# Optimization experiments

Measured on AMD Instinct MI355X. Metric: run time of the kernel, lower is better.

The kernel has to match this reference:

```python
import jax, jax.numpy as jnp
import numpy as np

B, C, H, W = 8, 96, 256, 256
PATCH, DIM, HEAD = 2, 384, 4
D = DIM // HEAD          # 96, minGRU feature dim
K = 2 * PATCH + 1        # 5, patch-embed kernel
GK = 3                   # positional conv kernel


def setup_inputs() -> dict:
    key = jax.random.key(0)
    ks = jax.random.split(key, 16)
    w = lambda k, shape: jax.random.normal(k, shape, jnp.float32) * 0.02
    return {
        'x': jax.random.normal(ks[0], (B, C, H, W), jnp.float32),
        'r_pw': w(ks[1], (DIM, C, K, K)),            # Conv2d weight (out,in,kh,kw)
        'r_pb': w(ks[2], (DIM,)),
        'c_pw': w(ks[3], (DIM, C, K, K)),
        'c_pb': w(ks[4], (DIM,)),
        'r_pe_w': w(ks[5], (DIM, DIM // C, GK, GK)),  # grouped conv, groups=C
        'r_pe_b': w(ks[6], (DIM,)),
        'c_pe_w': w(ks[7], (DIM, DIM // C, GK, GK)),
        'c_pe_b': w(ks[8], (DIM,)),
        'r_un_w': w(ks[9], (DIM, C, PATCH, PATCH)),   # ConvTranspose2d weight (in,out,kh,kw)
        'r_un_b': w(ks[10], (C,)),
        'c_un_w': w(ks[11], (DIM, C, PATCH, PATCH)),
        'c_un_b': w(ks[12], (C,)),
        'r_gru_w': w(ks[13], (D, 2 * D)),             # minGRU to_hidden_and_gate (no bias)
        'c_gru_w': w(ks[14], (D, 2 * D)),
    }


def _conv(x, w, b, stride, pad, groups=1):
    y = jax.lax.conv_general_dilated(
        x, w, (stride, stride), [(pad, pad), (pad, pad)],
        dimension_numbers=('NCHW', 'OIHW', 'NCHW'), feature_group_count=groups)
    return y + b[None, :, None, None]


def _min_gru(seq, w):
    # seq: (N, S, D); log-space parallel scan (heinsen scan), lucidrains minGRU
    hg = seq @ w                                  # (N, S, 2D)
    hidden, gate = jnp.split(hg, 2, axis=-1)
    log_coeffs = -jax.nn.softplus(gate)           # log(1 - z)
    log_z = -jax.nn.softplus(-gate)               # log z
    log_tilde_h = jnp.where(hidden >= 0,
                            jnp.log(jax.nn.relu(hidden) + 0.5),
                            -jax.nn.softplus(-hidden))
    a_star = jnp.cumsum(log_coeffs, axis=1)
    log_h = a_star + jax.lax.cumlogsumexp(log_z + log_tilde_h - a_star, axis=1)
    return jnp.exp(log_h)


def _unpatch(x, w, b):
    # ConvTranspose2d with kernel==stride==PATCH, pad=0: pure block expansion
    Bq, Ci, Hp, Wp = x.shape
    y = jnp.einsum('bchw,copq->bohpwq', x, w).reshape(Bq, w.shape[1], Hp * PATCH, Wp * PATCH)
    return y + b[None, :, None, None]


def reference(x, r_pw, r_pb, c_pw, c_pb, r_pe_w, r_pe_b, c_pe_w, c_pe_b,
              r_un_w, r_un_b, c_un_w, c_un_b, r_gru_w, c_gru_w):
    r = _conv(x, r_pw, r_pb, PATCH, PATCH)        # (B, DIM, Hp, Wp)
    c = _conv(x, c_pw, c_pb, PATCH, PATCH)
    r_pe = _conv(r, r_pe_w, r_pe_b, 1, 1, groups=C)
    c_pe = _conv(c, c_pe_w, c_pe_b, 1, 1, groups=C)
    Bq, _, Hp, Wp = r.shape
    # row scan: (B,head,D,Hp,Wp) -> (B,head,Wp,Hp,D) -> scan over Hp
    r = r.reshape(Bq, HEAD, D, Hp, Wp).transpose(0, 1, 4, 3, 2).reshape(-1, Hp, D)
    # col scan: (B,head,D,Hp,Wp) -> (B,head,Hp,Wp,D) -> scan over Wp
    c = c.reshape(Bq, HEAD, D, Hp, Wp).transpose(0, 1, 3, 4, 2).reshape(-1, Wp, D)
    r = _min_gru(r, r_gru_w)
    c = _min_gru(c, c_gru_w)
    r = r.reshape(Bq, HEAD, Wp, Hp, D).transpose(0, 1, 4, 3, 2).reshape(Bq, DIM, Hp, Wp)
    c = c.reshape(Bq, HEAD, Hp, Wp, D).transpose(0, 1, 4, 2, 3).reshape(Bq, DIM, Hp, Wp)
    return _unpatch(r + r_pe, r_un_w, r_un_b) + _unpatch(c + c_pe, c_un_w, c_un_b)
```

## Files before the change

### kernel.cpp

```cpp
#include <hip/hip_runtime.h>
#include <stdint.h>
#include <stdio.h>

typedef __attribute__((ext_vector_type(8))) short short8;
typedef __attribute__((ext_vector_type(4))) float f32x4;
typedef __attribute__((ext_vector_type(2))) float f32x2;
typedef __attribute__((ext_vector_type(4))) unsigned int u32x4;
typedef __attribute__((ext_vector_type(4))) unsigned short u16x4;

#define DEV static __device__ __forceinline__

DEV unsigned short f2bf(float f){
  unsigned u = __float_as_uint(f);
  u += 0x7FFFu + ((u >> 16) & 1u);
  return (unsigned short)(u >> 16);
}
DEV float bf2f(unsigned short h){ return __uint_as_float(((unsigned)h) << 16); }

__global__ __launch_bounds__(256) void k_xt(const float* __restrict__ x,
                                            unsigned short* __restrict__ xt){
  int bid = blockIdx.x;
  int wq = bid & 3, h = (bid >> 2) & 255, b = bid >> 10;
  int w0 = wq * 64;
  __shared__ unsigned short s[64 * 104];
  int t = threadIdx.x;
  int wl = t & 63, cq = t >> 6;
  const float* xp = x + ((size_t)b * 96 * 256 + h) * 256 + w0 + wl;
  #pragma unroll
  for (int i = 0; i < 24; ++i){
    int c = cq + i * 4;
    s[wl * 104 + c] = f2bf(xp[(size_t)c * 65536]);
  }
  __syncthreads();
  unsigned short* dst = xt + (((size_t)b * 260 + h + 2) * 260 + (w0 + 2)) * 128;
  #pragma unroll
  for (int p = 0; p < 3; ++p){
    int i = t + p * 256;
    int w = i / 12, ch = i % 12;
    u32x4 v = *(const u32x4*)&s[w * 104 + ch * 8];
    *(u32x4*)&dst[(size_t)w * 128 + ch * 8] = v;
  }
}

__global__ __launch_bounds__(256) void k_pack(const float* __restrict__ rpw, const float* __restrict__ cpw,
    const float* __restrict__ runw, const float* __restrict__ cunw,
    const float* __restrict__ runb, const float* __restrict__ cunb,
    const float* __restrict__ rgw,  const float* __restrict__ cgw,
    unsigned short* __restrict__ A2, unsigned short* __restrict__ Aun,
    unsigned short* __restrict__ Agr, float* __restrict__ bun){
  int tid = blockIdx.x * 256 + threadIdx.x;
  const int NA2 = 768 * 2400, NUN = 384 * 768, NGR = 2 * 192 * 96;
  if (tid < NA2){
    int oc = tid / 2400, r = tid % 2400;
    int kh = r / 480, kw = (r / 96) % 5, ic = r % 96;
    const float* W = oc < 384 ? rpw : cpw;
    int o = oc < 384 ? oc : oc - 384;
    A2[tid] = f2bf(W[(((size_t)o * 96 + ic) * 5 + kh) * 5 + kw]);
  } else if (tid < NA2 + NUN){
    int i = tid - NA2;
    int m = i / 768, ci = i % 768;
    int co = m >> 2, p = (m >> 1) & 1, q = m & 1;
    const float* W = ci < 384 ? runw : cunw;
    int c = ci < 384 ? ci : ci - 384;
    Aun[i] = f2bf(W[(((size_t)c * 96 + co) * 2 + p) * 2 + q]);
  } else if (tid < NA2 + NUN + NGR){
    int i = tid - NA2 - NUN;
    int side = i / 18432, r = i % 18432;
    int m = r / 96, k = r % 96;
    const float* W = side ? cgw : rgw;
    Agr[i] = f2bf(W[k * 192 + m]);
  } else if (tid < NA2 + NUN + NGR + 96){
    int co = tid - NA2 - NUN - NGR;
    bun[co] = runb[co] + cunb[co];
  }
}

__global__ __launch_bounds__(512) void k_conv(const unsigned short* __restrict__ xt,
    const unsigned short* __restrict__ A2,
    const float* __restrict__ rpb, const float* __restrict__ cpb,
    unsigned short* __restrict__ cl){
  __shared__ char lds[162240];
  const int ASZ = 26624;
  const int BOFF = 53248;
  const int BPITCH = 27248;
  const int BITEMS = 6288;
  int t = threadIdx.x, lane = t & 63;
  int wid = t >> 6, mw = wid >> 2, nw = wid & 3;
  int wl = lane & 15, cg = lane >> 4;
  int bid = blockIdx.x;
  int xcd = bid & 7, rr = bid >> 3;
  int mt = rr % 6, pgrp = rr / 6;
  int p = pgrp * 8 + xcd;
  int wq = p & 1, hq = (p >> 1) & 31, b = p >> 6;
  int ho0 = hq * 4, wo0 = wq * 64;
  int M0 = mt * 128;

  int a_oc = t >> 2, a_q = t & 3;
  const unsigned short* Aoc = A2 + (size_t)(M0 + a_oc) * 2400 + a_q * 24;
  char* Adst = lds + a_oc * 208 + a_q * 48;

  f32x4 acc[4][4];
  #pragma unroll
  for (int i = 0; i < 4; ++i)
    #pragma unroll
    for (int j = 0; j < 4; ++j) acc[i][j] = (f32x4){0.f, 0.f, 0.f, 0.f};

  u32x4 aR[3], bR[13];
  #pragma unroll
  for (int c = 0; c < 3; ++c) aR[c] = *(const u32x4*)(Aoc + c * 8);
  #pragma unroll
  for (int it = 0; it < 13; ++it){
    int i = t + it * 512;
    if (i < BITEMS){
      int row = i / 1572, j = i % 1572, col = j / 12, ch = j % 12;
      bR[it] = *(const u32x4*)&xt[(((size_t)b * 260 + 2 * ho0 + 2 * row) * 260 + 2 * wo0 + col) * 128 + ch * 8];
    }
  }
  #pragma unroll
  for (int c = 0; c < 3; ++c) *(u32x4*)(Adst + c * 16) = aR[c];
  #pragma unroll
  for (int it = 0; it < 13; ++it){
    int i = t + it * 512;
    if (i < BITEMS){
      int row = i / 1572, j = i % 1572, col = j / 12, ch = j % 12;
      *(u32x4*)(lds + BOFF + row * BPITCH + col * 208 + ch * 16) = bR[it];
    }
  }
  __syncthreads();

  int cur = 0;
  for (int kh = 0; kh < 5; ++kh){
    #pragma unroll
    for (int kw = 0; kw < 5; ++kw){
      bool last = (kh == 4 && kw == 4);
      bool khb  = (kw == 4 && kh < 4);
      if (!last){
        int nkh = kh + (kw == 4 ? 1 : 0), nkw = (kw == 4 ? 0 : kw + 1);
        const unsigned short* As = Aoc + (nkh * 5 + nkw) * 96;
        #pragma unroll
        for (int c = 0; c < 3; ++c) aR[c] = *(const u32x4*)(As + c * 8);
      }
      if (khb){
        #pragma unroll
        for (int it = 0; it < 13; ++it){
          int i = t + it * 512;
          if (i < BITEMS){
            int row = i / 1572, j = i % 1572, col = j / 12, ch = j % 12;
            bR[it] = *(const u32x4*)&xt[(((size_t)b * 260 + 2 * ho0 + 2 * row + kh + 1) * 260 + 2 * wo0 + col) * 128 + ch * 8];
          }
        }
      }
      {
        char* Ab = lds + cur * ASZ;
        int col = 32 * nw + 2 * wl + kw;
        #pragma unroll
        for (int ics = 0; ics < 3; ++ics){
          short8 af[4], bfr[4];
          #pragma unroll
          for (int mf = 0; mf < 4; ++mf)
            af[mf] = *(const short8*)(Ab + (mw * 64 + mf * 16 + wl) * 208 + ics * 64 + cg * 16);
          #pragma unroll
          for (int nf = 0; nf < 4; ++nf)
            bfr[nf] = *(const short8*)(lds + BOFF + nf * BPITCH + col * 208 + (ics * 4 + cg) * 16);
          #pragma unroll
          for (int mf = 0; mf < 4; ++mf)
            #pragma unroll
            for (int nf = 0; nf < 4; ++nf)
              acc[mf][nf] = __builtin_amdgcn_mfma_f32_16x16x32_bf16(af[mf], bfr[nf], acc[mf][nf], 0, 0, 0);
        }
      }
      if (khb) __syncthreads();
      if (!last){
        #pragma unroll
        for (int c = 0; c < 3; ++c) *(u32x4*)(Adst + (cur ^ 1) * ASZ + c * 16) = aR[c];
        if (khb){
          #pragma unroll
          for (int it = 0; it < 13; ++it){
            int i = t + it * 512;
            if (i < BITEMS){
              int row = i / 1572, j = i % 1572, col = j / 12, ch = j % 12;
              *(u32x4*)(lds + BOFF + row * BPITCH + col * 208 + ch * 16) = bR[it];
            }
          }
        }
        __syncthreads();
        cur ^= 1;
      }
    }
  }
  __syncthreads();
  unsigned short* S = (unsigned short*)lds;
  #pragma unroll
  for (int mf = 0; mf < 4; ++mf)
    #pragma unroll
    for (int nf = 0; nf < 4; ++nf){
      int wol = nw * 16 + wl;
      int pxl = nf * 64 + wol;
      int sw8 = (pxl & 7) << 3;
      #pragma unroll
      for (int j = 0; j < 4; ++j){
        int ocl = mw * 64 + mf * 16 + cg * 4 + j;
        int oc = M0 + ocl;
        float v = acc[mf][nf][j] + (oc < 384 ? rpb[oc] : cpb[oc - 384]);
        S[pxl * 128 + (ocl ^ sw8)] = f2bf(v);
      }
    }
  __syncthreads();
  #pragma unroll
  for (int it = 0; it < 8; ++it){
    int i = t + it * 512;
    int pxl = i >> 4, ch = i & 15;
    int chs = ch ^ (pxl & 7);
    int ho = ho0 + (pxl >> 6), wo = wo0 + (pxl & 63);
    u32x4 v = *(const u32x4*)&S[pxl * 128 + chs * 8];
    *(u32x4*)&cl[(((size_t)b * 128 + ho) * 128 + wo) * 768 + M0 + ch * 8] = v;
  }
}

__global__ __launch_bounds__(256) void k_pe(const unsigned short* __restrict__ cl,
    const float* __restrict__ rpew, const float* __restrict__ cpew,
    const float* __restrict__ rpeb, const float* __restrict__ cpeb,
    unsigned short* __restrict__ sum){
  __shared__ unsigned short si[340 * 52];
  __shared__ float sw[48 * 36];
  __shared__ float sb[48];
  int bid = blockIdx.x;
  int wq = bid & 3, hq = (bid >> 2) & 15, slab = (bid >> 6) & 15, b = bid >> 10;
  int ch0 = slab * 48, hp0 = hq * 8, wp0 = wq * 32;
  int t = threadIdx.x;
  for (int i = t; i < 48 * 36; i += 256){
    int ocl = i / 36, r = i % 36;
    int oc = ch0 + ocl;
    const float* W = oc < 384 ? rpew : cpew;
    int o = oc < 384 ? oc : oc - 384;
    sw[i] = W[(size_t)o * 36 + r];
  }
  if (t < 48){
    int oc = ch0 + t;
    sb[t] = oc < 384 ? rpeb[oc] : cpeb[oc - 384];
  }
  for (int i = t; i < 340 * 24; i += 256){
    int pix = i / 24, c2 = i % 24;
    int r2 = pix / 34, cc = pix % 34;
    int hp = hp0 - 1 + r2, wp = wp0 - 1 + cc;
    unsigned v = 0;
    if (hp >= 0 && hp < 128 && wp >= 0 && wp < 128)
      v = *(const unsigned*)&cl[((size_t)b * 16384 + hp * 128 + wp) * 768 + ch0 + c2 * 2];
    *(unsigned*)&si[pix * 52 + c2 * 2] = v;
  }
  __syncthreads();
  int hpl = t >> 5, wpl = t & 31;
  unsigned int outp[24];
  #pragma unroll
  for (int g = 0; g < 12; ++g){
    float o0 = sb[g * 4], o1 = sb[g * 4 + 1], o2 = sb[g * 4 + 2], o3 = sb[g * 4 + 3];
    #pragma unroll
    for (int dh = 0; dh < 3; ++dh)
      #pragma unroll
      for (int dw = 0; dw < 3; ++dw){
        int pix = (hpl + dh) * 34 + (wpl + dw);
        u16x4 v = *(const u16x4*)&si[pix * 52 + g * 4];
        float x0 = bf2f(v[0]), x1 = bf2f(v[1]), x2 = bf2f(v[2]), x3 = bf2f(v[3]);
        int r = dh * 3 + dw;
        o0 = fmaf(sw[(g*4+0)*36 + 0*9 + r], x0, o0); o0 = fmaf(sw[(g*4+0)*36 + 1*9 + r], x1, o0);
        o0 = fmaf(sw[(g*4+0)*36 + 2*9 + r], x2, o0); o0 = fmaf(sw[(g*4+0)*36 + 3*9 + r], x3, o0);
        o1 = fmaf(sw[(g*4+1)*36 + 0*9 + r], x0, o1); o1 = fmaf(sw[(g*4+1)*36 + 1*9 + r], x1, o1);
        o1 = fmaf(sw[(g*4+1)*36 + 2*9 + r], x2, o1); o1 = fmaf(sw[(g*4+1)*36 + 3*9 + r], x3, o1);
        o2 = fmaf(sw[(g*4+2)*36 + 0*9 + r], x0, o2); o2 = fmaf(sw[(g*4+2)*36 + 1*9 + r], x1, o2);
        o2 = fmaf(sw[(g*4+2)*36 + 2*9 + r], x2, o2); o2 = fmaf(sw[(g*4+2)*36 + 3*9 + r], x3, o2);
        o3 = fmaf(sw[(g*4+3)*36 + 0*9 + r], x0, o3); o3 = fmaf(sw[(g*4+3)*36 + 1*9 + r], x1, o3);
        o3 = fmaf(sw[(g*4+3)*36 + 2*9 + r], x2, o3); o3 = fmaf(sw[(g*4+3)*36 + 3*9 + r], x3, o3);
      }
    outp[g * 2]     = (unsigned)f2bf(o0) | ((unsigned)f2bf(o1) << 16);
    outp[g * 2 + 1] = (unsigned)f2bf(o2) | ((unsigned)f2bf(o3) << 16);
  }
  size_t obase = (((size_t)b * 128 + hp0 + hpl) * 128 + wp0 + wpl) * 768 + ch0;
  #pragma unroll
  for (int c6 = 0; c6 < 6; ++c6){
    u32x4 v = { outp[c6 * 4], outp[c6 * 4 + 1], outp[c6 * 4 + 2], outp[c6 * 4 + 3] };
    *(u32x4*)&sum[obase + c6 * 8] = v;
  }
}

__global__ __launch_bounds__(256) void k_gruf(const unsigned short* __restrict__ cl,
    const unsigned short* __restrict__ Agr, unsigned short* __restrict__ sum){
  __shared__ char lds[78848];
  const int AOFF = 0, BOFF2 = 39936, HOFF = 53248;
  int t = threadIdx.x, lane = t & 63, wid = t >> 6;
  int wl = lane & 15, cg = lane >> 4;
  int bid = blockIdx.x;
  int cb = bid & 7, head = (bid >> 3) & 3, b = (bid >> 5) & 7, side = bid >> 8;
  size_t clbase = ((size_t)b * 16384) * 768 + side * 384 + head * 96;
  for (int i = t; i < 2304; i += 256){
    int m = i / 12, c = i % 12;
    u32x4 v = *(const u32x4*)&Agr[((size_t)side * 192 + m) * 96 + c * 8];
    *(u32x4*)(lds + AOFF + m * 208 + c * 16) = v;
  }
  for (int i = t; i < 768; i += 256){
    int px = i / 12, c = i % 12;
    int s = px >> 4, xl = px & 15;
    int xg = cb * 16 + xl;
    int pxg = side ? (xg * 128 + s) : (s * 128 + xg);
    u32x4 v = *(const u32x4*)&cl[clbase + (size_t)pxg * 768 + c * 8];
    *(u32x4*)(lds + BOFF2 + px * 208 + c * 16) = v;
  }
  int s_chain = t & 15, s_dg = t >> 4;
  float h[8];
  #pragma unroll
  for (int k = 0; k < 8; ++k) h[k] = 0.f;
  __syncthreads();

  for (int ch = 0; ch < 32; ++ch){
    int s0 = ch * 4;
    f32x4 acc[12];
    #pragma unroll
    for (int i = 0; i < 12; ++i) acc[i] = (f32x4){0.f, 0.f, 0.f, 0.f};
    #pragma unroll
    for (int ks = 0; ks < 3; ++ks){
      short8 bf = *(const short8*)(lds + BOFF2 + (wid * 16 + wl) * 208 + ks * 64 + cg * 16);
      #pragma unroll
      for (int mf = 0; mf < 12; ++mf){
        short8 af = *(const short8*)(lds + AOFF + (mf * 16 + wl) * 208 + ks * 64 + cg * 16);
        acc[mf] = __builtin_amdgcn_mfma_f32_16x16x32_bf16(af, bf, acc[mf], 0, 0, 0);
      }
    }
    {
      int px = wid * 16 + wl;
      #pragma unroll
      for (int mf = 0; mf < 12; ++mf){
        unsigned p0 = (unsigned)f2bf(acc[mf][0]) | ((unsigned)f2bf(acc[mf][1]) << 16);
        unsigned p1 = (unsigned)f2bf(acc[mf][2]) | ((unsigned)f2bf(acc[mf][3]) << 16);
        unsigned long long pp = (unsigned long long)p0 | ((unsigned long long)p1 << 32);
        *(unsigned long long*)(lds + HOFF + px * 400 + (mf * 16 + cg * 4) * 2) = pp;
      }
    }
    __syncthreads();
    u32x4 nb[3];
    if (ch < 31){
      int sn = (ch + 1) * 4;
      #pragma unroll
      for (int it = 0; it < 3; ++it){
        int i = t + it * 256;
        int px = i / 12, c = i % 12;
        int s = px >> 4, xl = px & 15;
        int xg = cb * 16 + xl;
        int pxg = side ? (xg * 128 + (sn + s)) : ((sn + s) * 128 + xg);
        nb[it] = *(const u32x4*)&cl[clbase + (size_t)pxg * 768 + c * 8];
      }
    }
    if (s_dg < 12){
      #pragma unroll
      for (int s = 0; s < 4; ++s){
        int px = s * 16 + s_chain;
        short8 hid8 = *(const short8*)(lds + HOFF + px * 400 + s_dg * 16);
        short8 gat8 = *(const short8*)(lds + HOFF + px * 400 + 192 + s_dg * 16);
        int xg = cb * 16 + s_chain;
        int pxg = side ? (xg * 128 + (s0 + s)) : ((s0 + s) * 128 + xg);
        unsigned short* sp = (unsigned short*)&sum[clbase + (size_t)pxg * 768 + s_dg * 8];
        u32x4 sv = *(u32x4*)sp;
        unsigned short* svp = (unsigned short*)&sv;
        #pragma unroll
        for (int k = 0; k < 8; ++k){
          float hid = bf2f((unsigned short)hid8[k]);
          float gat = bf2f((unsigned short)gat8[k]);
          float z  = 1.f / (1.f + __expf(-gat));
          float th = hid >= 0.f ? hid + 0.5f : 1.f / (1.f + __expf(-hid));
          h[k] += z * (th - h[k]);
          svp[k] = f2bf(bf2f(svp[k]) + h[k]);
        }
        *(u32x4*)sp = sv;
      }
    }
    if (ch < 31){
      #pragma unroll
      for (int it = 0; it < 3; ++it){
        int i = t + it * 256;
        int px = i / 12, c = i % 12;
        *(u32x4*)(lds + BOFF2 + px * 208 + c * 16) = nb[it];
      }
    }
    __syncthreads();
  }
}

__global__ __launch_bounds__(256) void k_unpatch(const unsigned short* __restrict__ sum,
    const unsigned short* __restrict__ Aun, const float* __restrict__ bun,
    float* __restrict__ out){
  __shared__ char lds[53248];
  int t = threadIdx.x, lane = t & 63;
  int wid = t >> 6, mw = wid >> 1, nw = wid & 1;
  int bid = blockIdx.x;
  int xcd = bid & 7, rr = bid >> 3;
  int mt = rr % 3, pgrp = rr / 3;
  int M0 = mt * 128;
  size_t N0 = (size_t)(pgrp * 8 + xcd) * 128;
  f32x4 acc[4][4];
  #pragma unroll
  for (int i = 0; i < 4; ++i)
    #pragma unroll
    for (int j = 0; j < 4; ++j) acc[i][j] = (f32x4){0.f, 0.f, 0.f, 0.f};
  for (int kc = 0; kc < 8; ++kc){
    __syncthreads();
    for (int i = t; i < 1536; i += 256){
      int m = i / 12, c = i % 12;
      u32x4 v = *(const u32x4*)&Aun[(size_t)(M0 + m) * 768 + kc * 96 + c * 8];
      *(u32x4*)(lds + m * 208 + c * 16) = v;
    }
    for (int i = t; i < 1536; i += 256){
      int px = i / 12, c = i % 12;
      u32x4 v = *(const u32x4*)&sum[(N0 + px) * 768 + kc * 96 + c * 8];
      *(u32x4*)(lds + 26624 + px * 208 + c * 16) = v;
    }
    __syncthreads();
    #pragma unroll
    for (int ks = 0; ks < 3; ++ks){
      short8 af[4], bfr[4];
      #pragma unroll
      for (int mf = 0; mf < 4; ++mf)
        af[mf] = *(const short8*)(lds + (mw * 64 + mf * 16 + (lane & 15)) * 208 + ks * 64 + (lane >> 4) * 16);
      #pragma unroll
      for (int nf = 0; nf < 4; ++nf)
        bfr[nf] = *(const short8*)(lds + 26624 + (nw * 64 + nf * 16 + (lane & 15)) * 208 + ks * 64 + (lane >> 4) * 16);
      #pragma unroll
      for (int mf = 0; mf < 4; ++mf)
        #pragma unroll
        for (int nf = 0; nf < 4; ++nf)
          acc[mf][nf] = __builtin_amdgcn_mfma_f32_16x16x32_bf16(af[mf], bfr[nf], acc[mf][nf], 0, 0, 0);
    }
  }
  #pragma unroll
  for (int mf = 0; mf < 4; ++mf)
    #pragma unroll
    for (int nf = 0; nf < 4; ++nf){
      int m = M0 + mw * 64 + mf * 16 + (lane >> 4) * 4;
      int co = m >> 2;
      size_t px = N0 + nw * 64 + nf * 16 + (lane & 15);
      int b = (int)(px >> 14); int pxl = (int)(px & 16383);
      int hp = pxl >> 7, wp = pxl & 127;
      float bias = bun[co];
      f32x2 v01 = { acc[mf][nf][0] + bias, acc[mf][nf][1] + bias };
      f32x2 v23 = { acc[mf][nf][2] + bias, acc[mf][nf][3] + bias };
      size_t ob = (((size_t)b * 96 + co) * 256 + 2 * hp) * 256 + 2 * wp;
      *(f32x2*)&out[ob]       = v01;
      *(f32x2*)&out[ob + 256] = v23;
    }
}

extern "C" void kernel_launch(void* const* d_in, const int* in_sizes, int n_in,
                              void* d_out, int out_size, void* d_ws, size_t ws_size,
                              hipStream_t stream){
  (void)in_sizes; (void)n_in; (void)out_size;
  const float* x    = (const float*)d_in[0];
  const float* rpw  = (const float*)d_in[1];
  const float* rpb  = (const float*)d_in[2];
  const float* cpw  = (const float*)d_in[3];
  const float* cpb  = (const float*)d_in[4];
  const float* rpew = (const float*)d_in[5];
  const float* rpeb = (const float*)d_in[6];
  const float* cpew = (const float*)d_in[7];
  const float* cpeb = (const float*)d_in[8];
  const float* runw = (const float*)d_in[9];
  const float* runb = (const float*)d_in[10];
  const float* cunw = (const float*)d_in[11];
  const float* cunb = (const float*)d_in[12];
  const float* rgw  = (const float*)d_in[13];
  const float* cgw  = (const float*)d_in[14];

  char* ws = (char*)d_ws;
  const size_t SZ_XT   = (size_t)8 * 260 * 260 * 128 * 2;
  const size_t OFF_A2  = SZ_XT;
  const size_t SZ_A2   = (size_t)768 * 2400 * 2;
  const size_t OFF_AUN = OFF_A2 + SZ_A2;
  const size_t SZ_AUN  = (size_t)384 * 768 * 2;
  const size_t OFF_AGR = OFF_AUN + SZ_AUN;
  const size_t SZ_AGR  = (size_t)2 * 192 * 96 * 2;
  const size_t OFF_BUN = OFF_AGR + SZ_AGR;
  const size_t OFF_HG  = ((OFF_BUN + 384) + 255) & ~(size_t)255;
  const size_t SZ_PL   = (size_t)8 * 768 * 128 * 128 * 2;
  const size_t OFF_CL  = OFF_HG + SZ_PL;
  const size_t OFF_SUM = OFF_CL + SZ_PL;
  const size_t NEED    = OFF_SUM + SZ_PL;
  if (ws_size < NEED){
    fprintf(stderr, "kernel_launch: ws_size %zu < needed %zu\n", ws_size, NEED);
    return;
  }
  unsigned short* xt  = (unsigned short*)(ws);
  unsigned short* A2  = (unsigned short*)(ws + OFF_A2);
  unsigned short* Aun = (unsigned short*)(ws + OFF_AUN);
  unsigned short* Agr = (unsigned short*)(ws + OFF_AGR);
  float*          bun = (float*)(ws + OFF_BUN);
  unsigned short* cl  = (unsigned short*)(ws + OFF_CL);
  unsigned short* sum = (unsigned short*)(ws + OFF_SUM);
  float* out = (float*)d_out;

  hipMemsetAsync(xt, 0, SZ_XT, stream);
  k_xt  <<<dim3(8192),    dim3(256), 0, stream>>>(x, xt);
  k_pack<<<dim3(8497),    dim3(256), 0, stream>>>(rpw, cpw, runw, cunw, runb, cunb, rgw, cgw, A2, Aun, Agr, bun);
  k_conv<<<dim3(3072),    dim3(512), 0, stream>>>(xt, A2, rpb, cpb, cl);
  k_pe  <<<dim3(8192),    dim3(256), 0, stream>>>(cl, rpew, cpew, rpeb, cpeb, sum);
  k_gruf<<<dim3(512),     dim3(256), 0, stream>>>(cl, Agr, sum);
  k_unpatch<<<dim3(3072), dim3(256), 0, stream>>>(sum, Aun, bun, out);
}
```

Baseline: 1.486 ms.

## Zero only xt halo and register-prefetch next K chunk in unpatch GEMM

Replaces the full-buffer memset of the padded transposed input with a small kernel that zeros only the 2-pixel halo border, so the interior is written once by k_xt instead of twice. In k_unpatch, the next K chunk of A and B tiles is loaded into registers while the MFMAs for the current chunk run, then written to LDS between barriers, overlapping global loads with compute. The prefetch raises register pressure by holding twelve 16-byte vectors per thread, and correctness relies on the halo kernel covering every border cell (and all 128 channel slots) that the conv reads.

New measurement: 1.428 ms. 3.9% less time.

```diff
diff --git a/kernel.cpp b/kernel.cpp
--- a/kernel.cpp
+++ b/kernel.cpp
@@ -16,6 +16,26 @@
   return (unsigned short)(u >> 16);
 }
 DEV float bf2f(unsigned short h){ return __uint_as_float(((unsigned)h) << 16); }
+
+__global__ __launch_bounds__(256) void k_halo(unsigned short* __restrict__ xt){
+  int tid = blockIdx.x * 256 + threadIdx.x;
+  int ch = tid & 15;
+  int r = tid >> 4;
+  int k = r % 2064, b = r / 2064;
+  int row, col;
+  if (k < 1040){
+    int rr = k / 260;
+    row = rr < 2 ? rr : 256 + rr;
+    col = k % 260;
+  } else {
+    int k2 = k - 1040;
+    row = 2 + (k2 >> 2);
+    int cc = k2 & 3;
+    col = cc < 2 ? cc : 256 + cc;
+  }
+  u32x4 z = {0u, 0u, 0u, 0u};
+  *(u32x4*)&xt[(((size_t)b * 260 + row) * 260 + col) * 128 + ch * 8] = z;
+}
 
 __global__ __launch_bounds__(256) void k_xt(const float* __restrict__ x,
                                             unsigned short* __restrict__ xt){
@@ -399,19 +419,34 @@
   for (int i = 0; i < 4; ++i)
     #pragma unroll
     for (int j = 0; j < 4; ++j) acc[i][j] = (f32x4){0.f, 0.f, 0.f, 0.f};
+
+  int s_m = t / 2, s_c6 = (t & 1) * 6;
+  const unsigned short* Arow = Aun + (size_t)(M0 + s_m) * 768 + s_c6 * 8;
+  const unsigned short* Brow = sum + (N0 + s_m) * 768 + s_c6 * 8;
+  char* Adst = lds + s_m * 208 + s_c6 * 16;
+  char* Bdst = lds + 26624 + s_m * 208 + s_c6 * 16;
+
+  u32x4 aRg[6], bRg[6];
+  #pragma unroll
+  for (int c = 0; c < 6; ++c){
+    aRg[c] = *(const u32x4*)(Arow + c * 8);
+    bRg[c] = *(const u32x4*)(Brow + c * 8);
+  }
+  #pragma unroll
+  for (int c = 0; c < 6; ++c){
+    *(u32x4*)(Adst + c * 16) = aRg[c];
+    *(u32x4*)(Bdst + c * 16) = bRg[c];
+  }
+  __syncthreads();
+
   for (int kc = 0; kc < 8; ++kc){
-    __syncthreads();
-    for (int i = t; i < 1536; i += 256){
-      int m = i / 12, c = i % 12;
-      u32x4 v = *(const u32x4*)&Aun[(size_t)(M0 + m) * 768 + kc * 96 + c * 8];
-      *(u32x4*)(lds + m * 208 + c * 16) = v;
-    }
-    for (int i = t; i < 1536; i += 256){
-      int px = i / 12, c = i % 12;
-      u32x4 v = *(const u32x4*)&sum[(N0 + px) * 768 + kc * 96 + c * 8];
-      *(u32x4*)(lds + 26624 + px * 208 + c * 16) = v;
-    }
-    __syncthreads();
+    if (kc < 7){
+      #pragma unroll
+      for (int c = 0; c < 6; ++c){
+        aRg[c] = *(const u32x4*)(Arow + (kc + 1) * 96 + c * 8);
+        bRg[c] = *(const u32x4*)(Brow + (kc + 1) * 96 + c * 8);
+      }
+    }
     #pragma unroll
     for (int ks = 0; ks < 3; ++ks){
       short8 af[4], bfr[4];
@@ -426,6 +461,15 @@
         #pragma unroll
         for (int nf = 0; nf < 4; ++nf)
           acc[mf][nf] = __builtin_amdgcn_mfma_f32_16x16x32_bf16(af[mf], bfr[nf], acc[mf][nf], 0, 0, 0);
+    }
+    if (kc < 7){
+      __syncthreads();
+      #pragma unroll
+      for (int c = 0; c < 6; ++c){
+        *(u32x4*)(Adst + c * 16) = aRg[c];
+        *(u32x4*)(Bdst + c * 16) = bRg[c];
+      }
+      __syncthreads();
     }
   }
   #pragma unroll
@@ -493,7 +537,7 @@
   unsigned short* sum = (unsigned short*)(ws + OFF_SUM);
   float* out = (float*)d_out;
 
-  hipMemsetAsync(xt, 0, SZ_XT, stream);
+  k_halo<<<dim3(1032),    dim3(256), 0, stream>>>(xt);
   k_xt  <<<dim3(8192),    dim3(256), 0, stream>>>(x, xt);
   k_pack<<<dim3(8497),    dim3(256), 0, stream>>>(rpw, cpw, runw, cunw, runb, cunb, rgw, cgw, A2, Aun, Agr, bun);
   k_conv<<<dim3(3072),    dim3(512), 0, stream>>>(xt, A2, rpb, cpb, cl);
```
